# Kernel optimization log

Hardware: AMD Instinct MI355X
Metric: run time of the kernel (lower is better)

Reference implementation:

```python
import jax, jax.numpy as jnp
import numpy as np

B, S, D = 4, 4096, 256


def setup_inputs() -> dict:
    key = jax.random.key(0)
    ks = jax.random.split(key, 8)
    scale = 1.0 / np.sqrt(D)
    inp = {
        "q": jax.random.normal(ks[0], (B, S, D), jnp.float32),
        "k": jax.random.normal(ks[1], (B, S, D), jnp.float32),
        "v": jax.random.normal(ks[2], (B, S, D), jnp.float32),
        # additive mask: 1 where attention is disallowed (causal), broadcast over batch
        "mask": jnp.triu(jnp.ones((S, S), jnp.float32), k=1)[None, :, :],
        "Wq": jax.random.normal(ks[3], (D, D), jnp.float32) * scale,
        "bq": jnp.zeros((D,), jnp.float32),
        "Wk": jax.random.normal(ks[4], (D, D), jnp.float32) * scale,
        "bk": jnp.zeros((D,), jnp.float32),
        "Wv": jax.random.normal(ks[5], (D, D), jnp.float32) * scale,
        "bv": jnp.zeros((D,), jnp.float32),
        "Wo": jax.random.normal(ks[6], (D, D), jnp.float32) * scale,
        "bo": jnp.zeros((D,), jnp.float32),
    }
    return inp


def reference(q, k, v, mask, Wq, bq, Wk, bk, Wv, bv, Wo, bo):
    # Dense projections (Keras Dense: x @ W + b)
    qp = q @ Wq + bq  # [B,S,D]
    kp = k @ Wk + bk
    vp = v @ Wv + bv
    dk = jnp.asarray(qp.shape[-1], qp.dtype)
    # scaled dot-product attention, materialized scores as in the source
    logits = jnp.einsum("bqd,bkd->bqk", qp, kp) / jnp.sqrt(dk)  # [B,S,S]
    logits = logits + mask * (-1e9)
    attn = jax.nn.softmax(logits, axis=-1)  # [B,S,S]
    ctx = jnp.einsum("bqk,bkd->bqd", attn, vp)  # [B,S,D]
    z = ctx @ Wo + bo
    return z, attn
```

## Files before the change

kernel.cpp:

```cpp
#include <hip/hip_runtime.h>


typedef unsigned short u16;
typedef __attribute__((ext_vector_type(8))) short short8;
typedef __attribute__((ext_vector_type(4))) float f32x4;

struct __align__(8) us4 { u16 x, y, z, w; };

#define SEQ 4096
#define DIM 256

__device__ __forceinline__ u16 f2bf(float f) {
  unsigned int u = __float_as_uint(f);
  u += 0x7fffu + ((u >> 16) & 1u);
  return (u16)(u >> 16);
}
__device__ __forceinline__ float bf2f(u16 u) {
  return __uint_as_float(((unsigned int)u) << 16);
}

__device__ __forceinline__ void cp16(const void* g, void* l) {
  __builtin_amdgcn_global_load_lds((const __attribute__((address_space(1))) void*)g,
                                   (__attribute__((address_space(3))) void*)l, 16, 0, 0);
}

__global__ void k_wt(const float* __restrict__ Wq, const float* __restrict__ Wk,
                     const float* __restrict__ Wv, const float* __restrict__ Wo,
                     u16* __restrict__ wt) {
  __shared__ float t[32][33];
  const float* W = blockIdx.z == 0 ? Wq : blockIdx.z == 1 ? Wk : blockIdx.z == 2 ? Wv : Wo;
  u16* out = wt + (size_t)blockIdx.z * 65536;
  int n0 = blockIdx.x * 32, k0 = blockIdx.y * 32;
  int tx = threadIdx.x, ty = threadIdx.y;
  for (int i = 0; i < 4; i++)
    t[ty + i * 8][tx] = W[(size_t)(k0 + ty + i * 8) * 256 + n0 + tx];
  __syncthreads();
  for (int i = 0; i < 4; i++)
    out[(size_t)(n0 + ty + i * 8) * 256 + k0 + tx] = f2bf(t[tx][ty + i * 8]);
}

__global__ void k_pgemm3(const float* __restrict__ qin, const float* __restrict__ kin,
                         const float* __restrict__ vin, const u16* __restrict__ wtall,
                         const float* __restrict__ bq, const float* __restrict__ bk,
                         const float* __restrict__ bv,
                         u16* __restrict__ qp, u16* __restrict__ kp,
                         u16* __restrict__ vpt) {
  __shared__ __align__(16) char smem[34816];
  const int z = blockIdx.z;
  const float* A = z == 0 ? qin : z == 1 ? kin : vin;
  const u16* Wt = wtall + (size_t)z * 65536;
  const float* bias = z == 0 ? bq : z == 1 ? bk : bv;
  u16* outp = z == 0 ? qp : z == 1 ? kp : vpt;
  const bool TRANS = (z == 2);

  u16* Asm = (u16*)smem;
  u16* Bsm = Asm + 4096;
  u16* tb = (u16*)smem;
  const int tid = threadIdx.x;
  const int lane = tid & 63, w = tid >> 6;
  const int wr = w >> 1, wc = w & 1;
  const int quad = lane >> 4, m16 = lane & 15;
  const int m0 = blockIdx.y * 128, n0 = blockIdx.x * 128;

  f32x4 zero = {0.f, 0.f, 0.f, 0.f};
  f32x4 acc[4][4];
  for (int i = 0; i < 4; i++)
    for (int j = 0; j < 4; j++) acc[i][j] = zero;

  for (int kk = 0; kk < 8; ++kk) {
    const int k0 = kk * 32;
    for (int h = 0; h < 2; ++h) {
      int c = tid + h * 256;
      int row = c >> 2, sub = c & 3;
      cp16(Wt + (size_t)(n0 + row) * 256 + k0 + sub * 8, Bsm + c * 8);
    }
    for (int h = 0; h < 4; ++h) {
      int idx = h * 256 + tid;
      int row = idx >> 3, q4 = idx & 7;
      float4 a4 = *(const float4*)(A + (size_t)(m0 + row) * 256 + k0 + q4 * 4);
      us4 o;
      o.x = f2bf(a4.x); o.y = f2bf(a4.y); o.z = f2bf(a4.z); o.w = f2bf(a4.w);
      *(us4*)(Asm + row * 32 + q4 * 4) = o;
    }
    __syncthreads();
    short8 a[4], b[4];
    for (int i = 0; i < 4; ++i)
      a[i] = *(const short8*)(Asm + (wr * 64 + i * 16 + m16) * 32 + quad * 8);
    for (int j = 0; j < 4; ++j)
      b[j] = *(const short8*)(Bsm + (wc * 64 + j * 16 + m16) * 32 + quad * 8);
    for (int i = 0; i < 4; ++i)
      for (int j = 0; j < 4; ++j)
        acc[i][j] = __builtin_amdgcn_mfma_f32_16x16x32_bf16(a[i], b[j], acc[i][j], 0, 0, 0);
    __syncthreads();
  }

  if (!TRANS) {
    for (int j = 0; j < 4; ++j) {
      int gn = n0 + wc * 64 + j * 16 + m16;
      float bvx = bias[gn];
      for (int i = 0; i < 4; ++i) {
        int gm = m0 + wr * 64 + i * 16 + quad * 4;
        for (int r = 0; r < 4; ++r)
          outp[(size_t)(gm + r) * 256 + gn] = f2bf(acc[i][j][r] + bvx);
      }
    }
  } else {
    for (int j = 0; j < 4; ++j) {
      int cn = wc * 64 + j * 16 + m16;
      float bvx = bias[n0 + cn];
      for (int i = 0; i < 4; ++i) {
        int rm = wr * 64 + i * 16 + quad * 4;
        us4 o;
        o.x = f2bf(acc[i][j][0] + bvx); o.y = f2bf(acc[i][j][1] + bvx);
        o.z = f2bf(acc[i][j][2] + bvx); o.w = f2bf(acc[i][j][3] + bvx);
        *(us4*)(tb + cn * 136 + rm) = o;
      }
    }
    __syncthreads();
    int b = m0 >> 12, s0 = m0 & 4095;
    u16* dst = outp + ((size_t)b << 20);
    for (int it = 0; it < 8; ++it) {
      int idx = it * 256 + tid;
      int n = idx >> 4, m8 = idx & 15;
      short8 v8 = *(const short8*)(tb + n * 136 + m8 * 8);
      *(short8*)(dst + (size_t)(n0 + n) * 4096 + s0 + m8 * 8) = v8;
    }
  }
}

__global__ void k_qk(const u16* __restrict__ qp, const u16* __restrict__ kp,
                     u16* __restrict__ eb, float* __restrict__ attn,
                     float* __restrict__ ps) {
  int lin = blockIdx.x + (blockIdx.y << 5) + (blockIdx.z << 10);
  int wid = (lin & 7) * 512 + (lin >> 3);
  const int kt = wid & 31, qt = (wid >> 5) & 31, bz = wid >> 10;
  const int tid = threadIdx.x;
  const int q0 = qt * 128, k0t = kt * 128;

  if (kt > qt) {
    float* attnb = attn + ((size_t)bz << 24);
    f32x4 z4 = {0.f, 0.f, 0.f, 0.f};
    for (int s = 0; s < 16; ++s) {
      int idx = tid + s * 256;
      int row = idx >> 5, c4 = idx & 31;
      __builtin_nontemporal_store(z4,
          (f32x4*)(attnb + (size_t)(q0 + row) * 4096 + k0t + c4 * 4));
    }
    return;
  }

  __shared__ __align__(16) char smem[34816];
  u16* Asm = (u16*)smem;
  u16* Bsm = Asm + 4096;
  u16* epi = (u16*)smem;
  __shared__ float prow[2][128];

  const int lane = tid & 63, w = tid >> 6;
  const int wr = w >> 1, wc = w & 1;
  const int quad = lane >> 4, m16 = lane & 15;
  const u16* Ab = qp + ((size_t)bz << 20);
  const u16* Bb = kp + ((size_t)bz << 20);

  f32x4 zero = {0.f, 0.f, 0.f, 0.f};
  f32x4 acc[4][4];
  for (int i = 0; i < 4; i++)
    for (int j = 0; j < 4; j++) acc[i][j] = zero;

  for (int kk = 0; kk < 8; ++kk) {
    const int k0 = kk * 32;
    for (int h = 0; h < 2; ++h) {
      int c = tid + h * 256;
      int row = c >> 2, sub = c & 3;
      cp16(Ab + (size_t)(q0 + row) * 256 + k0 + sub * 8, Asm + c * 8);
      cp16(Bb + (size_t)(k0t + row) * 256 + k0 + sub * 8, Bsm + c * 8);
    }
    __syncthreads();
    short8 a[4], b[4];
    for (int i = 0; i < 4; ++i)
      a[i] = *(const short8*)(Asm + (wr * 64 + i * 16 + m16) * 32 + quad * 8);
    for (int j = 0; j < 4; ++j)
      b[j] = *(const short8*)(Bsm + (wc * 64 + j * 16 + m16) * 32 + quad * 8);
    for (int i = 0; i < 4; ++i)
      for (int j = 0; j < 4; ++j)
        acc[i][j] = __builtin_amdgcn_mfma_f32_16x16x32_bf16(a[i], b[j], acc[i][j], 0, 0, 0);
    __syncthreads();
  }

  float rs[4][4];
  for (int i = 0; i < 4; i++)
    for (int r = 0; r < 4; r++) rs[i][r] = 0.f;
  for (int i = 0; i < 4; ++i) {
    int gq = q0 + wr * 64 + i * 16 + quad * 4;
    for (int j = 0; j < 4; ++j) {
      int gk = k0t + wc * 64 + j * 16 + m16;
      for (int r = 0; r < 4; ++r) {
        float e = (gk <= gq + r) ? __expf(acc[i][j][r] * 0.0625f) : 0.f;
        acc[i][j][r] = e;
        rs[i][r] += e;
      }
    }
  }
  for (int off = 1; off < 16; off <<= 1)
    for (int i = 0; i < 4; ++i)
      for (int r = 0; r < 4; ++r) rs[i][r] += __shfl_xor(rs[i][r], off, 64);
  if (m16 == 0)
    for (int i = 0; i < 4; ++i)
      for (int r = 0; r < 4; ++r)
        prow[wc][wr * 64 + i * 16 + quad * 4 + r] = rs[i][r];

  for (int i = 0; i < 4; ++i)
    for (int j = 0; j < 4; ++j) {
      int rl = wr * 64 + i * 16 + quad * 4;
      int cl = wc * 64 + j * 16 + m16;
      for (int r = 0; r < 4; ++r) epi[(rl + r) * 136 + cl] = f2bf(acc[i][j][r]);
    }
  __syncthreads();

  u16* ebt = eb + ((size_t)bz * 528 + (size_t)(qt * (qt + 1) / 2 + kt)) * 16384;
  for (int it = 0; it < 8; ++it) {
    int idx = it * 256 + tid;
    int row = idx >> 4, m8 = idx & 15;
    short8 v8 = *(const short8*)(epi + row * 136 + m8 * 8);
    __builtin_nontemporal_store(v8, (short8*)(ebt + row * 128 + m8 * 8));
  }
  if (tid < 128)
    ps[(size_t)(bz * 32 + kt) * 4096 + q0 + tid] = prow[0][tid] + prow[1][tid];
}

__global__ void __launch_bounds__(512) k_pv2(const u16* __restrict__ eb,
                                             const u16* __restrict__ vpt,
                                             const float* __restrict__ ps,
                                             float* __restrict__ attn,
                                             float* __restrict__ ctxf) {
  int lin = blockIdx.x + (blockIdx.y << 2) + (blockIdx.z << 7);
  int wid = (lin & 7) * 64 + (lin >> 3);
  const int qt = wid & 31, kg = (wid >> 5) & 3, bz = wid >> 7;
  const int k_lo = kg * 1024;
  const int k_hi = min((qt + 1) * 128, k_lo + 1024);
  if (k_lo >= k_hi) return;

  __shared__ float inv_lds[128];

  const int tid = threadIdx.x;
  const int lane = tid & 63, w = tid >> 6;
  const int wr = w >> 2, wc = w & 3;
  const int quad = lane >> 4, m16 = lane & 15;
  const int q0 = qt * 128;
  const u16* ebq = eb + ((size_t)bz * 528 + (size_t)(qt * (qt + 1) / 2)) * 16384;
  float* attnb = attn + ((size_t)bz << 24);
  const u16* vb = vpt + ((size_t)bz << 20);

  if (tid < 128) {
    float s = 0.f;
    for (int kt = 0; kt <= qt; ++kt)
      s += ps[(size_t)(bz * 32 + kt) * 4096 + q0 + tid];
    inv_lds[tid] = 1.f / s;
  }
  __syncthreads();

  f32x4 zero = {0.f, 0.f, 0.f, 0.f};
  f32x4 acc[4][4];
  for (int i = 0; i < 4; i++)
    for (int j = 0; j < 4; j++) acc[i][j] = zero;

  for (int kt0 = k_lo; kt0 < k_hi; kt0 += 128) {
    const u16* ebtile = ebq + (size_t)(kt0 >> 7) * 16384;
    for (int p = 0; p < 4; ++p) {
      int idx = p * 512 + tid;
      int row = idx >> 4, c8 = idx & 15;
      short8 e8 = *(const short8*)(ebtile + row * 128 + c8 * 8);
      float ivr = inv_lds[row];
      f32x4 lo, hi;
      for (int t = 0; t < 4; ++t) lo[t] = bf2f((u16)e8[t]) * ivr;
      for (int t = 0; t < 4; ++t) hi[t] = bf2f((u16)e8[t + 4]) * ivr;
      float* dst = attnb + (size_t)(q0 + row) * 4096 + kt0 + c8 * 8;
      __builtin_nontemporal_store(lo, (f32x4*)dst);
      __builtin_nontemporal_store(hi, (f32x4*)(dst + 4));
    }
    for (int ks = 0; ks < 4; ++ks) {
      short8 a[4], b[4];
      for (int i = 0; i < 4; ++i)
        a[i] = *(const short8*)(ebtile + (wr * 64 + i * 16 + m16) * 128 + ks * 32 + quad * 8);
      for (int j = 0; j < 4; ++j)
        b[j] = *(const short8*)(vb + (size_t)(wc * 64 + j * 16 + m16) * 4096 + kt0 + ks * 32 + quad * 8);
      for (int i = 0; i < 4; ++i)
        for (int j = 0; j < 4; ++j)
          acc[i][j] = __builtin_amdgcn_mfma_f32_16x16x32_bf16(a[i], b[j], acc[i][j], 0, 0, 0);
    }
  }

  float* ctxs = ctxf + ((size_t)(kg * 4 + bz) << 20);
  for (int i = 0; i < 4; ++i) {
    int rl = wr * 64 + i * 16 + quad * 4;
    for (int j = 0; j < 4; ++j) {
      int gn = wc * 64 + j * 16 + m16;
      for (int r = 0; r < 4; ++r)
        ctxs[(size_t)(q0 + rl + r) * 256 + gn] = acc[i][j][r] * inv_lds[rl + r];
    }
  }
}

__global__ void k_cvt(const float* __restrict__ ctxf, u16* __restrict__ ctx) {
  size_t i4 = (size_t)blockIdx.x * 256 + threadIdx.x;
  int bz = (int)(i4 >> 18);
  size_t rem4 = i4 & (((size_t)1 << 18) - 1);
  int qrow = (int)(rem4 >> 6);
  int nact = (qrow >> 10) + 1;
  const float4* base = (const float4*)ctxf;
  float4 s = base[((size_t)bz << 18) + rem4];
  for (int kg = 1; kg < nact; ++kg) {
    float4 t = base[((size_t)(kg * 4 + bz) << 18) + rem4];
    s.x += t.x; s.y += t.y; s.z += t.z; s.w += t.w;
  }
  us4 o;
  o.x = f2bf(s.x); o.y = f2bf(s.y); o.z = f2bf(s.z); o.w = f2bf(s.w);
  ((us4*)ctx)[i4] = o;
}

template <bool OUT_BF16>
__global__ void k_gemm(const u16* __restrict__ A, const u16* __restrict__ Wt,
                       const float* __restrict__ bias, void* __restrict__ outp) {
  __shared__ u16 Asm[128 * 32];
  __shared__ u16 Bsm[128 * 32];
  const int tid = threadIdx.x;
  const int lane = tid & 63, w = tid >> 6;
  const int wr = w >> 1, wc = w & 1;
  const int quad = lane >> 4, m16 = lane & 15;
  const int m0 = blockIdx.y * 128, n0 = blockIdx.x * 128;

  f32x4 zero = {0.f, 0.f, 0.f, 0.f};
  f32x4 acc[4][4];
  for (int i = 0; i < 4; i++)
    for (int j = 0; j < 4; j++) acc[i][j] = zero;

  for (int kk = 0; kk < 8; ++kk) {
    const int k0 = kk * 32;
    for (int h = 0; h < 2; ++h) {
      int c = tid + h * 256;
      int row = c >> 2, sub = c & 3;
      cp16(A + (size_t)(m0 + row) * 256 + k0 + sub * 8, Asm + c * 8);
      cp16(Wt + (size_t)(n0 + row) * 256 + k0 + sub * 8, Bsm + c * 8);
    }
    __syncthreads();
    short8 a[4], b[4];
    for (int i = 0; i < 4; ++i)
      a[i] = *(const short8*)(Asm + (wr * 64 + i * 16 + m16) * 32 + quad * 8);
    for (int j = 0; j < 4; ++j)
      b[j] = *(const short8*)(Bsm + (wc * 64 + j * 16 + m16) * 32 + quad * 8);
    for (int i = 0; i < 4; ++i)
      for (int j = 0; j < 4; ++j)
        acc[i][j] = __builtin_amdgcn_mfma_f32_16x16x32_bf16(a[i], b[j], acc[i][j], 0, 0, 0);
    __syncthreads();
  }

  for (int j = 0; j < 4; ++j) {
    int gn = n0 + wc * 64 + j * 16 + m16;
    float bv = bias[gn];
    for (int i = 0; i < 4; ++i) {
      int gm = m0 + wr * 64 + i * 16 + quad * 4;
      for (int r = 0; r < 4; ++r) {
        float val = acc[i][j][r] + bv;
        if (OUT_BF16)
          ((u16*)outp)[(size_t)(gm + r) * 256 + gn] = f2bf(val);
        else
          ((float*)outp)[(size_t)(gm + r) * 256 + gn] = val;
      }
    }
  }
}

extern "C" void kernel_launch(void* const* d_in, const int* in_sizes, int n_in,
                              void* d_out, int out_size, void* d_ws, size_t ws_size,
                              hipStream_t stream) {
  const float* q  = (const float*)d_in[0];
  const float* k  = (const float*)d_in[1];
  const float* v  = (const float*)d_in[2];
  const float* Wq = (const float*)d_in[4];
  const float* bq = (const float*)d_in[5];
  const float* Wk = (const float*)d_in[6];
  const float* bk = (const float*)d_in[7];
  const float* Wv = (const float*)d_in[8];
  const float* bv = (const float*)d_in[9];
  const float* Wo = (const float*)d_in[10];
  const float* bo = (const float*)d_in[11];

  const size_t MD = (size_t)16384 * 256;
  u16* qp  = (u16*)d_ws;
  u16* kp  = qp + MD;
  u16* vpt = kp + MD;
  u16* ctx = vpt + MD;
  u16* wt  = ctx + MD;
  float* ps   = (float*)(wt + 4 * 65536);
  float* ctxf = ps + (size_t)4 * 32 * 4096;
  u16* eb = (u16*)(ctxf + (size_t)16 * 1024 * 1024);

  float* zout = (float*)d_out;
  float* attn = zout + (size_t)4 * 4096 * 256;

  k_wt<<<dim3(8, 8, 4), dim3(32, 8), 0, stream>>>(Wq, Wk, Wv, Wo, wt);
  k_pgemm3<<<dim3(2, 128, 3), 256, 0, stream>>>(q, k, v, wt, bq, bk, bv, qp, kp, vpt);
  k_qk<<<dim3(32, 32, 4), 256, 0, stream>>>(qp, kp, eb, attn, ps);
  k_pv2<<<dim3(4, 32, 4), 512, 0, stream>>>(eb, vpt, ps, attn, ctxf);
  k_cvt<<<4096, 256, 0, stream>>>(ctxf, ctx);
  k_gemm<false><<<dim3(2, 128), 256, 0, stream>>>(ctx, wt + 3 * 65536, bo, zout);
}
```

Baseline: 595.7 us.

## Stage P·V tiles through swizzled double-buffered LDS and balance causal K splits

The P·V kernel now splits each query tile's output columns into two halves. Its causal K range is divided evenly into four groups by tile count instead of fixed 1024-wide chunks, which balances work across blocks. The E and V tiles are staged through double-buffered, XOR-swizzled LDS with register prefetch, replacing direct global loads for the MFMA operands. This doubles the grid and halves per-block accumulators, which aims to improve occupancy and load balance. The trade-off is that each E tile is read twice, once per column half, and the reduction kernel is updated to match the new group layout.

New measurement: 502.2 us. 15.7% less time.

```diff
diff --git a/kernel.cpp b/kernel.cpp
--- a/kernel.cpp
+++ b/kernel.cpp
@@ -232,13 +232,16 @@
                                              const float* __restrict__ ps,
                                              float* __restrict__ attn,
                                              float* __restrict__ ctxf) {
-  int lin = blockIdx.x + (blockIdx.y << 2) + (blockIdx.z << 7);
-  int wid = (lin & 7) * 64 + (lin >> 3);
-  const int qt = wid & 31, kg = (wid >> 5) & 3, bz = wid >> 7;
-  const int k_lo = kg * 1024;
-  const int k_hi = min((qt + 1) * 128, k_lo + 1024);
-  if (k_lo >= k_hi) return;
-
+  int lin = blockIdx.x + (blockIdx.y << 3) + (blockIdx.z << 8);
+  int wid = (lin & 7) * 128 + (lin >> 3);
+  const int nh = wid & 1, kg = (wid >> 1) & 3;
+  const int qt = (wid >> 3) & 31, bz = wid >> 8;
+  const int nt_lo = (kg * (qt + 1)) >> 2;
+  const int nt_hi = ((kg + 1) * (qt + 1)) >> 2;
+  if (nt_lo >= nt_hi) return;
+
+  __shared__ u16 A_lds[2][128 * 64];
+  __shared__ u16 B_lds[2][128 * 64];
   __shared__ float inv_lds[128];
 
   const int tid = threadIdx.x;
@@ -248,7 +251,7 @@
   const int q0 = qt * 128;
   const u16* ebq = eb + ((size_t)bz * 528 + (size_t)(qt * (qt + 1) / 2)) * 16384;
   float* attnb = attn + ((size_t)bz << 24);
-  const u16* vb = vpt + ((size_t)bz << 20);
+  const u16* vb = vpt + ((size_t)bz << 20) + (size_t)nh * 128 * 4096;
 
   if (tid < 128) {
     float s = 0.f;
@@ -256,44 +259,84 @@
       s += ps[(size_t)(bz * 32 + kt) * 4096 + q0 + tid];
     inv_lds[tid] = 1.f / s;
   }
+
+  short8 arg0, arg1, brg0, brg1;
+  const int srow0 = tid >> 3, srow1 = (512 + tid) >> 3;
+  const int sc = tid & 7;
+
+  auto stage_load = [&](int hh) {
+    int t0 = nt_lo + (hh >> 1), h = hh & 1;
+    const u16* tile = ebq + (size_t)t0 * 16384 + h * 64;
+    int kt0 = t0 * 128 + h * 64;
+    arg0 = *(const short8*)(tile + srow0 * 128 + sc * 8);
+    arg1 = *(const short8*)(tile + srow1 * 128 + sc * 8);
+    brg0 = *(const short8*)(vb + (size_t)srow0 * 4096 + kt0 + sc * 8);
+    brg1 = *(const short8*)(vb + (size_t)srow1 * 4096 + kt0 + sc * 8);
+  };
+  const int soff0 = srow0 * 64 + ((((sc << 4) ^ ((srow0 & 7) << 4))) >> 1);
+  const int soff1 = srow1 * 64 + ((((sc << 4) ^ ((srow1 & 7) << 4))) >> 1);
+  auto stage_write = [&](int buf) {
+    *(short8*)(A_lds[buf] + soff0) = arg0;
+    *(short8*)(A_lds[buf] + soff1) = arg1;
+    *(short8*)(B_lds[buf] + soff0) = brg0;
+    *(short8*)(B_lds[buf] + soff1) = brg1;
+  };
+
+  const int khalves = (nt_hi - nt_lo) * 2;
+  stage_load(0);
+  stage_write(0);
   __syncthreads();
 
   f32x4 zero = {0.f, 0.f, 0.f, 0.f};
-  f32x4 acc[4][4];
-  for (int i = 0; i < 4; i++)
-    for (int j = 0; j < 4; j++) acc[i][j] = zero;
-
-  for (int kt0 = k_lo; kt0 < k_hi; kt0 += 128) {
-    const u16* ebtile = ebq + (size_t)(kt0 >> 7) * 16384;
-    for (int p = 0; p < 4; ++p) {
-      int idx = p * 512 + tid;
-      int row = idx >> 4, c8 = idx & 15;
-      short8 e8 = *(const short8*)(ebtile + row * 128 + c8 * 8);
-      float ivr = inv_lds[row];
+  f32x4 acc[4][2];
+  for (int i = 0; i < 4; i++)
+    for (int j = 0; j < 2; j++) acc[i][j] = zero;
+
+  for (int hh = 0; hh < khalves; ++hh) {
+    const int buf = hh & 1;
+    if (hh + 1 < khalves) stage_load(hh + 1);
+
+    {
+      int rl = nh * 64 + (tid >> 3);
+      int c8 = tid & 7;
+      int lb = rl * 64 + ((((c8 << 4) ^ ((rl & 7) << 4))) >> 1);
+      short8 e8 = *(const short8*)(A_lds[buf] + lb);
+      float ivr = inv_lds[rl];
       f32x4 lo, hi;
       for (int t = 0; t < 4; ++t) lo[t] = bf2f((u16)e8[t]) * ivr;
       for (int t = 0; t < 4; ++t) hi[t] = bf2f((u16)e8[t + 4]) * ivr;
-      float* dst = attnb + (size_t)(q0 + row) * 4096 + kt0 + c8 * 8;
+      int kcol = (nt_lo + (hh >> 1)) * 128 + (hh & 1) * 64 + (c8 << 3);
+      float* dst = attnb + (size_t)(q0 + rl) * 4096 + kcol;
       __builtin_nontemporal_store(lo, (f32x4*)dst);
       __builtin_nontemporal_store(hi, (f32x4*)(dst + 4));
     }
-    for (int ks = 0; ks < 4; ++ks) {
-      short8 a[4], b[4];
+
+    for (int ks = 0; ks < 2; ++ks) {
+      short8 a[4], b[2];
+      for (int i = 0; i < 4; ++i) {
+        int row = wr * 64 + i * 16 + m16;
+        int xb = (ks * 64 + quad * 16) ^ ((row & 7) << 4);
+        a[i] = *(const short8*)(A_lds[buf] + row * 64 + (xb >> 1));
+      }
+      for (int j = 0; j < 2; ++j) {
+        int n = wc * 32 + j * 16 + m16;
+        int xb = (ks * 64 + quad * 16) ^ ((n & 7) << 4);
+        b[j] = *(const short8*)(B_lds[buf] + n * 64 + (xb >> 1));
+      }
       for (int i = 0; i < 4; ++i)
-        a[i] = *(const short8*)(ebtile + (wr * 64 + i * 16 + m16) * 128 + ks * 32 + quad * 8);
-      for (int j = 0; j < 4; ++j)
-        b[j] = *(const short8*)(vb + (size_t)(wc * 64 + j * 16 + m16) * 4096 + kt0 + ks * 32 + quad * 8);
-      for (int i = 0; i < 4; ++i)
-        for (int j = 0; j < 4; ++j)
+        for (int j = 0; j < 2; ++j)
           acc[i][j] = __builtin_amdgcn_mfma_f32_16x16x32_bf16(a[i], b[j], acc[i][j], 0, 0, 0);
     }
+
+    if (hh + 1 < khalves) stage_write(buf ^ 1);
+    __syncthreads();
   }
 
   float* ctxs = ctxf + ((size_t)(kg * 4 + bz) << 20);
   for (int i = 0; i < 4; ++i) {
     int rl = wr * 64 + i * 16 + quad * 4;
-    for (int j = 0; j < 4; ++j) {
-      int gn = wc * 64 + j * 16 + m16;
+    for (int j = 0; j < 2; ++j) {
+      int gn = nh * 128 + wc * 32 + j * 16 + m16;
       for (int r = 0; r < 4; ++r)
         ctxs[(size_t)(q0 + rl + r) * 256 + gn] = acc[i][j][r] * inv_lds[rl + r];
     }
@@ -305,12 +348,14 @@
   int bz = (int)(i4 >> 18);
   size_t rem4 = i4 & (((size_t)1 << 18) - 1);
   int qrow = (int)(rem4 >> 6);
-  int nact = (qrow >> 10) + 1;
+  int qt = qrow >> 7;
   const float4* base = (const float4*)ctxf;
-  float4 s = base[((size_t)bz << 18) + rem4];
-  for (int kg = 1; kg < nact; ++kg) {
-    float4 t = base[((size_t)(kg * 4 + bz) << 18) + rem4];
-    s.x += t.x; s.y += t.y; s.z += t.z; s.w += t.w;
+  float4 s = make_float4(0.f, 0.f, 0.f, 0.f);
+  for (int kg = 0; kg < 4; ++kg) {
+    if ((((kg + 1) * (qt + 1)) >> 2) > ((kg * (qt + 1)) >> 2)) {
+      float4 t = base[((size_t)(kg * 4 + bz) << 18) + rem4];
+      s.x += t.x; s.y += t.y; s.z += t.z; s.w += t.w;
+    }
   }
   us4 o;
   o.x = f2bf(s.x); o.y = f2bf(s.y); o.z = f2bf(s.z); o.w = f2bf(s.w);
@@ -400,7 +445,7 @@
   k_wt<<<dim3(8, 8, 4), dim3(32, 8), 0, stream>>>(Wq, Wk, Wv, Wo, wt);
   k_pgemm3<<<dim3(2, 128, 3), 256, 0, stream>>>(q, k, v, wt, bq, bk, bv, qp, kp, vpt);
   k_qk<<<dim3(32, 32, 4), 256, 0, stream>>>(qp, kp, eb, attn, ps);
-  k_pv2<<<dim3(4, 32, 4), 512, 0, stream>>>(eb, vpt, ps, attn, ctxf);
+  k_pv2<<<dim3(8, 32, 4), 512, 0, stream>>>(eb, vpt, ps, attn, ctxf);
   k_cvt<<<4096, 256, 0, stream>>>(ctxf, ctx);
   k_gemm<false><<<dim3(2, 128), 256, 0, stream>>>(ctx, wt + 3 * 65536, bo, zout);
 }
```
